# Kernel tuning notes

Hardware: AMD Instinct MI355X
Metric: run time of the kernel (lower is better)

Reference implementation:

```python
import jax, jax.numpy as jnp
import numpy as np

HID = 2048   # hidden_size
NH = 32      # num_heads (== num_kv_heads)
HD = 64      # head_dim
TH, TW = 8, 16     # tile sizes (tile numel 128, flex-attention block)
WH, WW = 16, 32    # window sizes in tokens
SCALE = 1.0 / np.sqrt(HD)


def _kv_tile_index(h_dim, w_dim):
    # Static tile-level sliding window (mirrors sliding_window_tile_2d mask_mod).
    Ht, Wt = h_dim // TH, w_dim // TW          # tile grid
    wh, ww = WH // TH, WW // TW                # window in tile units
    lr, rr = wh // 2, wh // 2 + (wh % 2 - 1)
    lc, rc = ww // 2, ww // 2 + (ww % 2 - 1)
    cr = np.clip(np.arange(Ht), lr, Ht - 1 - rr)   # clamped window center rows
    cc = np.clip(np.arange(Wt), lc, Wt - 1 - rc)
    rows = cr[:, None] + np.arange(-lr, rr + 1)[None, :]   # [Ht, wh]
    cols = cc[:, None] + np.arange(-lc, rc + 1)[None, :]   # [Wt, ww]
    idx = rows[:, None, :, None] * Wt + cols[None, :, None, :]  # [Ht,Wt,wh,ww]
    return idx.reshape(Ht * Wt, wh * ww)


def _tile_order(x, h_dim, w_dim):
    # seq layout (nth th ntw tw) -> [B, NH, n_tiles, TH*TW, HD]  (the einops rearrange)
    B, S, _ = x.shape
    nth, ntw = h_dim // TH, w_dim // TW
    x = x.reshape(B, nth, TH, ntw, TW, NH, HD)
    x = x.transpose(0, 5, 1, 3, 2, 4, 6)  # b h nth ntw th tw d
    return x.reshape(B, NH, nth * ntw, TH * TW, HD)


def setup_inputs() -> dict:
    key = jax.random.key(0)
    ks = jax.random.split(key, 5)
    B, hd, wd = 2, 64, 64
    S = hd * wd
    sc = 1.0 / np.sqrt(HID)
    return {
        "hidden_states": jax.random.normal(ks[0], (B, S, HID), jnp.float32),
        "Wq": jax.random.normal(ks[1], (HID, NH * HD), jnp.float32) * sc,
        "Wk": jax.random.normal(ks[2], (HID, NH * HD), jnp.float32) * sc,
        "Wv": jax.random.normal(ks[3], (HID, NH * HD), jnp.float32) * sc,
        "Wo": jax.random.normal(ks[4], (NH * HD, HID), jnp.float32) * sc,
        "h_dim": hd,
        "w_dim": wd,
    }


def reference(hidden_states, Wq, Wk, Wv, Wo, h_dim, w_dim):
    B, S, _ = hidden_states.shape
    q = _tile_order(hidden_states @ Wq, h_dim, w_dim)
    k = _tile_order(hidden_states @ Wk, h_dim, w_dim)
    v = _tile_order(hidden_states @ Wv, h_dim, w_dim)
    kv_tiles = jnp.asarray(_kv_tile_index(h_dim, w_dim))  # [T, nw] static
    T, nw = kv_tiles.shape
    tn = TH * TW
    # gather the allowed kv tiles per query tile (block-sparse structure)
    kg = k[:, :, kv_tiles].reshape(B, NH, T, nw * tn, HD)
    vg = v[:, :, kv_tiles].reshape(B, NH, T, nw * tn, HD)
    s = jnp.einsum('bhtqd,bhtkd->bhtqk', q, kg) * SCALE  # [B,H,T,128,nw*128]
    p = jax.nn.softmax(s, axis=-1)
    o = jnp.einsum('bhtqk,bhtkd->bhtqd', p, vg)
    # back to (nth th ntw tw) token order, then output projection
    nth, ntw = h_dim // TH, w_dim // TW
    o = o.reshape(B, NH, nth, ntw, TH, TW, HD)
    o = o.transpose(0, 2, 4, 3, 5, 1, 6).reshape(B, S, NH * HD)
    return o @ Wo
```

## Files before the change

kernel.cpp:

```cpp
#include <hip/hip_runtime.h>
#include <math.h>

typedef _Float16 f16;
typedef _Float16 f16x8 __attribute__((ext_vector_type(8)));
typedef float f32x4 __attribute__((ext_vector_type(4)));

#define K_HID 2048
#define N_SEQ 4096
#define N_BATCH 2
#define M_ROWS 8192

__device__ __forceinline__ void gl2lds16(const f16* g, f16* l) {
  auto gp = (const __attribute__((address_space(1))) unsigned*)(unsigned long long)(uintptr_t)g;
  auto lp = (__attribute__((address_space(3))) unsigned*)(unsigned)(uintptr_t)l;
  __builtin_amdgcn_global_load_lds(gp, lp, 16, 0, 0);
}

__global__ __launch_bounds__(256) void cvt_f32_to_f16(const float* __restrict__ x,
                                                      f16* __restrict__ y, int n) {
  int i = (blockIdx.x * 256 + threadIdx.x) * 8;
  if (i >= n) return;
  float4 a = *(const float4*)(x + i);
  float4 b = *(const float4*)(x + i + 4);
  f16x8 o;
  o[0] = (f16)a.x; o[1] = (f16)a.y; o[2] = (f16)a.z; o[3] = (f16)a.w;
  o[4] = (f16)b.x; o[5] = (f16)b.y; o[6] = (f16)b.z; o[7] = (f16)b.w;
  *(f16x8*)(y + i) = o;
}

__global__ __launch_bounds__(256) void transpose_cvt(const float* __restrict__ W0,
                                                     const float* __restrict__ W1,
                                                     const float* __restrict__ W2,
                                                     const float* __restrict__ W3,
                                                     f16* __restrict__ WT) {
  const float* W = (blockIdx.z == 0) ? W0 : (blockIdx.z == 1) ? W1
                 : (blockIdx.z == 2) ? W2 : W3;
  f16* Wt = WT + (size_t)blockIdx.z * K_HID * K_HID;
  __shared__ float tile[32][33];
  int bx = blockIdx.x * 32;
  int by = blockIdx.y * 32;
  int x = threadIdx.x & 31;
  int y = threadIdx.x >> 5;
  for (int i = 0; i < 32; i += 8)
    tile[y + i][x] = W[(size_t)(by + y + i) * K_HID + bx + x];
  __syncthreads();
  for (int i = 0; i < 32; i += 8)
    Wt[(size_t)(bx + y + i) * K_HID + by + x] = (f16)tile[x][y + i];
}

template <typename OutT>
__global__ __launch_bounds__(512, 2) void gemm_bt(const f16* __restrict__ A,
                                                  const f16* __restrict__ BtBase,
                                                  OutT* __restrict__ CBase,
                                                  int M, int N, int Kd,
                                                  size_t bzStride, size_t czStride) {
  const f16* Bt = BtBase + bzStride * blockIdx.z;
  OutT* C = CBase + czStride * blockIdx.z;
  __shared__ f16 sA[2][256 * 64];
  __shared__ f16 sB[2][256 * 64];
  int tid = threadIdx.x;
  int lane = tid & 63, wave = tid >> 6;
  int quad = lane >> 4, l16 = lane & 15;
  int mBase = blockIdx.y * 256, nBase = blockIdx.x * 256;
  int wm = (wave >> 2) * 128, wn = (wave & 3) * 64;

  f32x4 acc[8][4];
#pragma unroll
  for (int mf = 0; mf < 8; mf++)
#pragma unroll
    for (int nf = 0; nf < 4; nf++) acc[mf][nf] = (f32x4){0.f, 0.f, 0.f, 0.f};

  int r8 = lane >> 3;
  int csw = ((lane & 7) ^ r8) * 8;
  const f16* Ag = A + (size_t)(mBase + wave * 32 + r8) * Kd + csw;
  const f16* Bg = Bt + (size_t)(nBase + wave * 32 + r8) * Kd + csw;

  f16* lA0 = &sA[0][wave * 2048];
  f16* lA1 = &sA[1][wave * 2048];
  f16* lB0 = &sB[0][wave * 2048];
  f16* lB1 = &sB[1][wave * 2048];

#define STAGE_A(dst, t)                                                  \
  { _Pragma("unroll") for (int q = 0; q < 4; ++q)                        \
      gl2lds16(Ag + (size_t)(q * 8) * Kd + (size_t)(t) * 64, (dst) + q * 512); }
#define STAGE_B(dst, t)                                                  \
  { _Pragma("unroll") for (int q = 0; q < 4; ++q)                        \
      gl2lds16(Bg + (size_t)(q * 8) * Kd + (size_t)(t) * 64, (dst) + q * 512); }

  int aRow = (wm + l16) * 64;
  int bRow = (wn + l16) * 64;
  int c0 = (quad ^ (l16 & 7)) * 8;
  int c1 = c0 ^ 32;

  const int NT = Kd >> 6;
  STAGE_A(lA0, 0);
  STAGE_B(lB0, 0);

  const f16* sAc = &sA[0][0]; const f16* sAo = &sA[1][0];
  const f16* sBc = &sB[0][0]; const f16* sBo = &sB[1][0];
  f16* lAn = lA1; f16* lAo = lA0;
  f16* lBn = lB1; f16* lBo = lB0;

  for (int t = 0; t < NT; ++t) {
    if (t + 1 < NT) {
      STAGE_A(lAn, t + 1);
      asm volatile("s_waitcnt vmcnt(4)" ::: "memory");
    } else {
      asm volatile("s_waitcnt vmcnt(0)" ::: "memory");
    }
    __builtin_amdgcn_s_barrier();
    __builtin_amdgcn_sched_barrier(0);

    f16x8 bf[4][2], af[4][2];
#pragma unroll
    for (int nf = 0; nf < 4; nf++) {
      bf[nf][0] = *(const f16x8*)&sBc[bRow + nf * 1024 + c0];
      bf[nf][1] = *(const f16x8*)&sBc[bRow + nf * 1024 + c1];
    }
#pragma unroll
    for (int mf = 0; mf < 4; mf++) {
      af[mf][0] = *(const f16x8*)&sAc[aRow + mf * 1024 + c0];
      af[mf][1] = *(const f16x8*)&sAc[aRow + mf * 1024 + c1];
    }
    __builtin_amdgcn_s_setprio(1);
#pragma unroll
    for (int mf = 0; mf < 4; mf++)
#pragma unroll
      for (int nf = 0; nf < 4; nf++) {
        acc[mf][nf] = __builtin_amdgcn_mfma_f32_16x16x32_f16(af[mf][0], bf[nf][0], acc[mf][nf], 0, 0, 0);
        acc[mf][nf] = __builtin_amdgcn_mfma_f32_16x16x32_f16(af[mf][1], bf[nf][1], acc[mf][nf], 0, 0, 0);
      }
    __builtin_amdgcn_s_setprio(0);

    if (t + 1 < NT) STAGE_B(lBn, t + 1);

#pragma unroll
    for (int mf = 0; mf < 4; mf++) {
      af[mf][0] = *(const f16x8*)&sAc[aRow + 4096 + mf * 1024 + c0];
      af[mf][1] = *(const f16x8*)&sAc[aRow + 4096 + mf * 1024 + c1];
    }
    __builtin_amdgcn_s_setprio(1);
#pragma unroll
    for (int mf = 0; mf < 4; mf++)
#pragma unroll
      for (int nf = 0; nf < 4; nf++) {
        acc[mf + 4][nf] = __builtin_amdgcn_mfma_f32_16x16x32_f16(af[mf][0], bf[nf][0], acc[mf + 4][nf], 0, 0, 0);
        acc[mf + 4][nf] = __builtin_amdgcn_mfma_f32_16x16x32_f16(af[mf][1], bf[nf][1], acc[mf + 4][nf], 0, 0, 0);
      }
    __builtin_amdgcn_s_setprio(0);
    __builtin_amdgcn_sched_barrier(0);
    __builtin_amdgcn_s_barrier();

    { const f16* tt;
      tt = sAc; sAc = sAo; sAo = tt;
      tt = sBc; sBc = sBo; sBo = tt; }
    { f16* tt;
      tt = lAn; lAn = lAo; lAo = tt;
      tt = lBn; lBn = lBo; lBo = tt; }
  }
#undef STAGE_A
#undef STAGE_B

#pragma unroll
  for (int mf = 0; mf < 8; mf++) {
    int row = mBase + wm + mf * 16 + quad * 4;
#pragma unroll
    for (int nf = 0; nf < 4; nf++) {
      int col = nBase + wn + nf * 16 + l16;
      OutT* Cp = C + (size_t)row * N + col;
#pragma unroll
      for (int r = 0; r < 4; r++) Cp[(size_t)r * N] = (OutT)acc[mf][nf][r];
    }
  }
}

__global__ __launch_bounds__(256) void attn_kernel(const f16* __restrict__ Q,
                                                   const f16* __restrict__ Kg,
                                                   const f16* __restrict__ V,
                                                   f16* __restrict__ O) {
  __shared__ f16 sQ[128 * 72];
  __shared__ f16 sK[64 * 72];
  __shared__ f16 sVt[64 * 72];
  __shared__ f16 sP[128 * 72];

  int t = blockIdx.x, h = blockIdx.y, b = blockIdx.z;
  int nth_i = t >> 2, ntw_i = t & 3;
  int tid = threadIdx.x;
  int lane = tid & 63, wave = tid >> 6;
  int quad = lane >> 4, l16 = lane & 15;
  const size_t bstride = (size_t)N_SEQ * K_HID;
  const f16* Qb = Q + (size_t)b * bstride + h * 64;
  const f16* Kb = Kg + (size_t)b * bstride + h * 64;
  const f16* Vb = V + (size_t)b * bstride + h * 64;

  const float SC2 = 0.18033688f;

  for (int i = tid; i < 1024; i += 256) {
    int qr = i >> 3, dc = (i & 7) * 8;
    int s = (nth_i * 8 + (qr >> 4)) * 64 + ntw_i * 16 + (qr & 15);
    *(float4*)&sQ[qr * 72 + dc] = *(const float4*)&Qb[(size_t)s * K_HID + dc];
  }
  __syncthreads();

  f16x8 qf[2][2];
#pragma unroll
  for (int qs = 0; qs < 2; qs++)
#pragma unroll
    for (int kk = 0; kk < 2; kk++)
      qf[qs][kk] = *(const f16x8*)&sQ[(wave * 32 + qs * 16 + l16) * 72 + kk * 32 + quad * 8];

  f32x4 oacc[2][4];
#pragma unroll
  for (int qs = 0; qs < 2; qs++)
#pragma unroll
    for (int dt = 0; dt < 4; dt++) oacc[qs][dt] = (f32x4){0.f, 0.f, 0.f, 0.f};
  float mrow[2][4], lrow[2][4];
#pragma unroll
  for (int qs = 0; qs < 2; qs++)
#pragma unroll
    for (int r = 0; r < 4; r++) { mrow[qs][r] = -1e30f; lrow[qs][r] = 0.f; }

  int cr = min(max(nth_i, 1), 7);
  int cc = min(max(ntw_i, 1), 3);

  for (int c = 0; c < 8; c++) {
    int kt = c >> 1, half = c & 1;
    int ti = cr - 1 + (kt >> 1), tj = cc - 1 + (kt & 1);
    for (int i = tid; i < 512; i += 256) {
      int kl = i >> 3, dc = (i & 7) * 8;
      int kr = half * 64 + kl;
      int s = (ti * 8 + (kr >> 4)) * 64 + tj * 16 + (kr & 15);
      *(float4*)&sK[kl * 72 + dc] = *(const float4*)&Kb[(size_t)s * K_HID + dc];
      f16x8 vv = *(const f16x8*)&Vb[(size_t)s * K_HID + dc];
      int sw = kl ^ dc;
#pragma unroll
      for (int j = 0; j < 8; j++) sVt[(dc + j) * 72 + sw] = vv[j];
    }
    __syncthreads();

    f32x4 sacc[2][4];
#pragma unroll
    for (int qs = 0; qs < 2; qs++)
#pragma unroll
      for (int ks = 0; ks < 4; ks++) sacc[qs][ks] = (f32x4){0.f, 0.f, 0.f, 0.f};
#pragma unroll
    for (int ks = 0; ks < 4; ks++) {
      f16x8 kf0 = *(const f16x8*)&sK[(ks * 16 + l16) * 72 + quad * 8];
      f16x8 kf1 = *(const f16x8*)&sK[(ks * 16 + l16) * 72 + 32 + quad * 8];
#pragma unroll
      for (int qs = 0; qs < 2; qs++) {
        sacc[qs][ks] = __builtin_amdgcn_mfma_f32_16x16x32_f16(qf[qs][0], kf0, sacc[qs][ks], 0, 0, 0);
        sacc[qs][ks] = __builtin_amdgcn_mfma_f32_16x16x32_f16(qf[qs][1], kf1, sacc[qs][ks], 0, 0, 0);
      }
    }

#pragma unroll
    for (int qs = 0; qs < 2; qs++) {
#pragma unroll
      for (int r = 0; r < 4; r++) {
        float mx = fmaxf(fmaxf(sacc[qs][0][r], sacc[qs][1][r]),
                         fmaxf(sacc[qs][2][r], sacc[qs][3][r]));
        for (int d = 1; d < 16; d <<= 1) mx = fmaxf(mx, __shfl_xor(mx, d, 64));
        mx *= SC2;
        float mold = mrow[qs][r];
        float mnew = fmaxf(mold, mx);
        mrow[qs][r] = mnew;
        float alpha = exp2f(mold - mnew);
        lrow[qs][r] *= alpha;
#pragma unroll
        for (int dt = 0; dt < 4; dt++) oacc[qs][dt][r] *= alpha;
      }
#pragma unroll
      for (int ks = 0; ks < 4; ks++) {
#pragma unroll
        for (int r = 0; r < 4; r++) {
          float p = exp2f(sacc[qs][ks][r] * SC2 - mrow[qs][r]);
          lrow[qs][r] += p;
          sP[(wave * 32 + qs * 16 + quad * 4 + r) * 72 + ks * 16 + l16] = (f16)p;
        }
      }
    }
    __syncthreads();

#pragma unroll
    for (int kk = 0; kk < 2; kk++) {
      f16x8 pf[2];
#pragma unroll
      for (int qs = 0; qs < 2; qs++)
        pf[qs] = *(const f16x8*)&sP[(wave * 32 + qs * 16 + l16) * 72 + kk * 32 + quad * 8];
#pragma unroll
      for (int dt = 0; dt < 4; dt++) {
        int d = dt * 16 + l16;
        f16x8 vf = *(const f16x8*)&sVt[d * 72 + ((kk * 32 + quad * 8) ^ (d & 56))];
#pragma unroll
        for (int qs = 0; qs < 2; qs++)
          oacc[qs][dt] = __builtin_amdgcn_mfma_f32_16x16x32_f16(pf[qs], vf, oacc[qs][dt], 0, 0, 0);
      }
    }
    __syncthreads();
  }

  f16* Ob = O + (size_t)b * bstride + h * 64;
#pragma unroll
  for (int qs = 0; qs < 2; qs++) {
#pragma unroll
    for (int r = 0; r < 4; r++) {
      float l = lrow[qs][r];
      for (int d = 1; d < 16; d <<= 1) l += __shfl_xor(l, d, 64);
      float inv = 1.0f / l;
      int qr = wave * 32 + qs * 16 + quad * 4 + r;
      int s = (nth_i * 8 + (qr >> 4)) * 64 + ntw_i * 16 + (qr & 15);
#pragma unroll
      for (int dt = 0; dt < 4; dt++)
        Ob[(size_t)s * K_HID + dt * 16 + l16] = (f16)(oacc[qs][dt][r] * inv);
    }
  }
}

extern "C" void kernel_launch(void* const* d_in, const int* in_sizes, int n_in,
                              void* d_out, int out_size, void* d_ws, size_t ws_size,
                              hipStream_t stream) {
  const float* hs = (const float*)d_in[0];
  const float* Wq = (const float*)d_in[1];
  const float* Wk = (const float*)d_in[2];
  const float* Wv = (const float*)d_in[3];
  const float* Wo = (const float*)d_in[4];
  float* out = (float*)d_out;

  char* ws = (char*)d_ws;
  const size_t WELEM = (size_t)K_HID * K_HID;
  const size_t XELEM = (size_t)M_ROWS * K_HID;
  f16* WT = (f16*)ws;  ws += 4 * WELEM * sizeof(f16);
  f16* Xh = (f16*)ws;  ws += XELEM * sizeof(f16);
  f16* Qb = (f16*)ws;  ws += XELEM * sizeof(f16);
  f16* Kb = (f16*)ws;  ws += XELEM * sizeof(f16);
  f16* Vb = (f16*)ws;  ws += XELEM * sizeof(f16);
  f16* Ob = (f16*)ws;  ws += XELEM * sizeof(f16);

  cvt_f32_to_f16<<<(int)(XELEM / (256 * 8)), 256, 0, stream>>>(hs, Xh, (int)XELEM);
  transpose_cvt<<<dim3(64, 64, 4), 256, 0, stream>>>(Wq, Wk, Wv, Wo, WT);
  gemm_bt<f16><<<dim3(8, 32, 3), 512, 0, stream>>>(Xh, WT, Qb, M_ROWS, K_HID, K_HID,
                                                   WELEM, XELEM);
  attn_kernel<<<dim3(32, 32, 2), 256, 0, stream>>>(Qb, Kb, Vb, Ob);
  gemm_bt<float><<<dim3(8, 32, 1), 512, 0, stream>>>(Ob, WT + 3 * WELEM, out,
                                                     M_ROWS, K_HID, K_HID, 0, 0);
}
```

Baseline: 560.1 us.

## Restructure GEMM main loop into four-phase K-split pipeline with interleaved staging

Changes the GEMM's LDS layout from 64-wide swizzled rows to two 32-wide K halves. The main loop now runs four MFMA phases per K tile, each separated by barriers, with the next tile's A and B halves issued between phases so loads overlap compute more finely. The A fragments for all 8 m-fragments are held in registers, and B is reloaded in halves. The unswizzled 32-wide rows may cause LDS bank conflicts, and the extra barriers add synchronisation cost.

```diff
diff --git a/kernel.cpp b/kernel.cpp
--- a/kernel.cpp
+++ b/kernel.cpp
@@ -56,8 +56,8 @@
                                                   size_t bzStride, size_t czStride) {
   const f16* Bt = BtBase + bzStride * blockIdx.z;
   OutT* C = CBase + czStride * blockIdx.z;
-  __shared__ f16 sA[2][256 * 64];
-  __shared__ f16 sB[2][256 * 64];
+  __shared__ f16 sA[2 * 2 * 256 * 32];
+  __shared__ f16 sB[2 * 2 * 256 * 32];
   int tid = threadIdx.x;
   int lane = tid & 63, wave = tid >> 6;
   int quad = lane >> 4, l16 = lane & 15;
@@ -70,96 +70,101 @@
 #pragma unroll
     for (int nf = 0; nf < 4; nf++) acc[mf][nf] = (f32x4){0.f, 0.f, 0.f, 0.f};
 
-  int r8 = lane >> 3;
-  int csw = ((lane & 7) ^ r8) * 8;
-  const f16* Ag = A + (size_t)(mBase + wave * 32 + r8) * Kd + csw;
-  const f16* Bg = Bt + (size_t)(nBase + wave * 32 + r8) * Kd + csw;
-
-  f16* lA0 = &sA[0][wave * 2048];
-  f16* lA1 = &sA[1][wave * 2048];
-  f16* lB0 = &sB[0][wave * 2048];
-  f16* lB1 = &sB[1][wave * 2048];
-
-#define STAGE_A(dst, t)                                                  \
-  { _Pragma("unroll") for (int q = 0; q < 4; ++q)                        \
-      gl2lds16(Ag + (size_t)(q * 8) * Kd + (size_t)(t) * 64, (dst) + q * 512); }
-#define STAGE_B(dst, t)                                                  \
-  { _Pragma("unroll") for (int q = 0; q < 4; ++q)                        \
-      gl2lds16(Bg + (size_t)(q * 8) * Kd + (size_t)(t) * 64, (dst) + q * 512); }
-
-  int aRow = (wm + l16) * 64;
-  int bRow = (wn + l16) * 64;
-  int c0 = (quad ^ (l16 & 7)) * 8;
-  int c1 = c0 ^ 32;
+  int r4 = lane >> 2;
+  int kc = (lane & 3) * 8;
+  const f16* Ag = A + (size_t)(mBase + wave * 16 + r4) * Kd + kc;
+  const f16* Bg = Bt + (size_t)(nBase + wave * 16 + r4) * Kd + kc;
+
+#define STG(g, dstBase, kh, j, tt)                                           \
+  gl2lds16((g) + (size_t)((j) * 128) * Kd + (size_t)((tt) * 64 + (kh) * 32), \
+           (dstBase) + (kh) * 8192 + ((j) * 128 + wave * 16) * 32)
+
+  f16* cA = sA;          f16* nA = sA + 16384;
+  f16* cB = sB;          f16* nB = sB + 16384;
 
   const int NT = Kd >> 6;
-  STAGE_A(lA0, 0);
-  STAGE_B(lB0, 0);
-
-  const f16* sAc = &sA[0][0]; const f16* sAo = &sA[1][0];
-  const f16* sBc = &sB[0][0]; const f16* sBo = &sB[1][0];
-  f16* lAn = lA1; f16* lAo = lA0;
-  f16* lBn = lB1; f16* lBo = lB0;
+
+  STG(Ag, cA, 0, 0, 0); STG(Ag, cA, 0, 1, 0);
+  STG(Bg, cB, 0, 0, 0); STG(Bg, cB, 0, 1, 0);
+  STG(Ag, cA, 1, 0, 0); STG(Ag, cA, 1, 1, 0);
+  STG(Bg, cB, 1, 0, 0); STG(Bg, cB, 1, 1, 0);
+  asm volatile("s_waitcnt vmcnt(4)" ::: "memory");
+  __builtin_amdgcn_s_barrier();
+
+  int aOff = (wm + l16) * 32 + quad * 8;
+  int bOff = (wn + l16) * 32 + quad * 8;
 
   for (int t = 0; t < NT; ++t) {
-    if (t + 1 < NT) {
-      STAGE_A(lAn, t + 1);
-      asm volatile("s_waitcnt vmcnt(4)" ::: "memory");
-    } else {
-      asm volatile("s_waitcnt vmcnt(0)" ::: "memory");
-    }
-    __builtin_amdgcn_s_barrier();
+    const bool pre = (t + 1 < NT);
+    f16x8 af[8], bq[2];
+#pragma unroll
+    for (int mf = 0; mf < 8; mf++) af[mf] = *(const f16x8*)&cA[aOff + mf * 512];
+#pragma unroll
+    for (int nf = 0; nf < 2; nf++) bq[nf] = *(const f16x8*)&cB[bOff + nf * 512];
+    if (pre) { STG(Ag, nA, 0, 0, t + 1); STG(Ag, nA, 0, 1, t + 1); }
+    __builtin_amdgcn_s_barrier();
+    asm volatile("s_waitcnt lgkmcnt(0)" ::: "memory");
     __builtin_amdgcn_sched_barrier(0);
-
-    f16x8 bf[4][2], af[4][2];
-#pragma unroll
-    for (int nf = 0; nf < 4; nf++) {
-      bf[nf][0] = *(const f16x8*)&sBc[bRow + nf * 1024 + c0];
-      bf[nf][1] = *(const f16x8*)&sBc[bRow + nf * 1024 + c1];
-    }
-#pragma unroll
-    for (int mf = 0; mf < 4; mf++) {
-      af[mf][0] = *(const f16x8*)&sAc[aRow + mf * 1024 + c0];
-      af[mf][1] = *(const f16x8*)&sAc[aRow + mf * 1024 + c1];
-    }
     __builtin_amdgcn_s_setprio(1);
 #pragma unroll
-    for (int mf = 0; mf < 4; mf++)
-#pragma unroll
-      for (int nf = 0; nf < 4; nf++) {
-        acc[mf][nf] = __builtin_amdgcn_mfma_f32_16x16x32_f16(af[mf][0], bf[nf][0], acc[mf][nf], 0, 0, 0);
-        acc[mf][nf] = __builtin_amdgcn_mfma_f32_16x16x32_f16(af[mf][1], bf[nf][1], acc[mf][nf], 0, 0, 0);
-      }
+    for (int mf = 0; mf < 8; mf++)
+#pragma unroll
+      for (int nf = 0; nf < 2; nf++)
+        acc[mf][nf] = __builtin_amdgcn_mfma_f32_16x16x32_f16(af[mf], bq[nf], acc[mf][nf], 0, 0, 0);
     __builtin_amdgcn_s_setprio(0);
-
-    if (t + 1 < NT) STAGE_B(lBn, t + 1);
-
-#pragma unroll
-    for (int mf = 0; mf < 4; mf++) {
-      af[mf][0] = *(const f16x8*)&sAc[aRow + 4096 + mf * 1024 + c0];
-      af[mf][1] = *(const f16x8*)&sAc[aRow + 4096 + mf * 1024 + c1];
-    }
+    __builtin_amdgcn_s_barrier();
+#pragma unroll
+    for (int nf = 0; nf < 2; nf++) bq[nf] = *(const f16x8*)&cB[bOff + (nf + 2) * 512];
+    if (pre) { STG(Bg, nB, 0, 0, t + 1); STG(Bg, nB, 0, 1, t + 1); }
+    __builtin_amdgcn_s_barrier();
+    asm volatile("s_waitcnt lgkmcnt(0)" ::: "memory");
+    __builtin_amdgcn_sched_barrier(0);
     __builtin_amdgcn_s_setprio(1);
 #pragma unroll
-    for (int mf = 0; mf < 4; mf++)
-#pragma unroll
-      for (int nf = 0; nf < 4; nf++) {
-        acc[mf + 4][nf] = __builtin_amdgcn_mfma_f32_16x16x32_f16(af[mf][0], bf[nf][0], acc[mf + 4][nf], 0, 0, 0);
-        acc[mf + 4][nf] = __builtin_amdgcn_mfma_f32_16x16x32_f16(af[mf][1], bf[nf][1], acc[mf + 4][nf], 0, 0, 0);
-      }
+    for (int mf = 0; mf < 8; mf++)
+#pragma unroll
+      for (int nf = 0; nf < 2; nf++)
+        acc[mf][nf + 2] = __builtin_amdgcn_mfma_f32_16x16x32_f16(af[mf], bq[nf], acc[mf][nf + 2], 0, 0, 0);
     __builtin_amdgcn_s_setprio(0);
+    __builtin_amdgcn_s_barrier();
+    if (pre) asm volatile("s_waitcnt vmcnt(4)" ::: "memory");
+    else     asm volatile("s_waitcnt vmcnt(0)" ::: "memory");
+#pragma unroll
+    for (int mf = 0; mf < 8; mf++) af[mf] = *(const f16x8*)&cA[8192 + aOff + mf * 512];
+#pragma unroll
+    for (int nf = 0; nf < 2; nf++) bq[nf] = *(const f16x8*)&cB[8192 + bOff + (nf + 2) * 512];
+    if (pre) { STG(Ag, nA, 1, 0, t + 1); STG(Ag, nA, 1, 1, t + 1); }
+    __builtin_amdgcn_s_barrier();
+    asm volatile("s_waitcnt lgkmcnt(0)" ::: "memory");
     __builtin_amdgcn_sched_barrier(0);
-    __builtin_amdgcn_s_barrier();
-
-    { const f16* tt;
-      tt = sAc; sAc = sAo; sAo = tt;
-      tt = sBc; sBc = sBo; sBo = tt; }
-    { f16* tt;
-      tt = lAn; lAn = lAo; lAo = tt;
-      tt = lBn; lBn = lBo; lBo = tt; }
-  }
-#undef STAGE_A
-#undef STAGE_B
+    __builtin_amdgcn_s_setprio(1);
+#pragma unroll
+    for (int mf = 0; mf < 8; mf++)
+#pragma unroll
+      for (int nf = 0; nf < 2; nf++)
+        acc[mf][nf + 2] = __builtin_amdgcn_mfma_f32_16x16x32_f16(af[mf], bq[nf], acc[mf][nf + 2], 0, 0, 0);
+    __builtin_amdgcn_s_setprio(0);
+    __builtin_amdgcn_s_barrier();
+#pragma unroll
+    for (int nf = 0; nf < 2; nf++) bq[nf] = *(const f16x8*)&cB[8192 + bOff + nf * 512];
+    if (pre) { STG(Bg, nB, 1, 0, t + 1); STG(Bg, nB, 1, 1, t + 1); }
+    if (pre) asm volatile("s_waitcnt vmcnt(4)" ::: "memory");
+    else     asm volatile("s_waitcnt vmcnt(0)" ::: "memory");
+    __builtin_amdgcn_s_barrier();
+    asm volatile("s_waitcnt lgkmcnt(0)" ::: "memory");
+    __builtin_amdgcn_sched_barrier(0);
+    __builtin_amdgcn_s_setprio(1);
+#pragma unroll
+    for (int mf = 0; mf < 8; mf++)
+#pragma unroll
+      for (int nf = 0; nf < 2; nf++)
+        acc[mf][nf] = __builtin_amdgcn_mfma_f32_16x16x32_f16(af[mf], bq[nf], acc[mf][nf], 0, 0, 0);
+    __builtin_amdgcn_s_setprio(0);
+    __builtin_amdgcn_s_barrier();
+    f16* tA = cA; cA = nA; nA = tA;
+    f16* tB = cB; cB = nB; nB = tB;
+  }
+#undef STG
 
 #pragma unroll
   for (int mf = 0; mf < 8; mf++) {
```

Result: slower. 594.4 us (+6.1%).

## Transpose attention MFMA operands so softmax rows live per lane

Applied to the files above, without the earlier changes.

Swaps the A/B operands of the QK^T and PV MFMAs so each lane holds a query column rather than a row slice. Row max and sum then need only two cross-quad shuffles instead of four-step reductions per register, and P and O can be written as packed f16x4 vectors. The Q staging buffer is merged into the P buffer to save LDS, and the V transpose now writes packed f16x2 pairs. The change targets the attention kernel only; the GEMMs dominate total time, so the overall effect may be small.

```diff
diff --git a/kernel.cpp b/kernel.cpp
--- a/kernel.cpp
+++ b/kernel.cpp
@@ -2,6 +2,8 @@
 #include <math.h>
 
 typedef _Float16 f16;
+typedef _Float16 f16x2 __attribute__((ext_vector_type(2)));
+typedef _Float16 f16x4 __attribute__((ext_vector_type(4)));
 typedef _Float16 f16x8 __attribute__((ext_vector_type(8)));
 typedef float f32x4 __attribute__((ext_vector_type(4)));
 
@@ -178,10 +180,9 @@
                                                    const f16* __restrict__ Kg,
                                                    const f16* __restrict__ V,
                                                    f16* __restrict__ O) {
-  __shared__ f16 sQ[128 * 72];
   __shared__ f16 sK[64 * 72];
   __shared__ f16 sVt[64 * 72];
-  __shared__ f16 sP[128 * 72];
+  __shared__ f16 sPt[128 * 72];
 
   int t = blockIdx.x, h = blockIdx.y, b = blockIdx.z;
   int nth_i = t >> 2, ntw_i = t & 3;
@@ -198,7 +199,7 @@
   for (int i = tid; i < 1024; i += 256) {
     int qr = i >> 3, dc = (i & 7) * 8;
     int s = (nth_i * 8 + (qr >> 4)) * 64 + ntw_i * 16 + (qr & 15);
-    *(float4*)&sQ[qr * 72 + dc] = *(const float4*)&Qb[(size_t)s * K_HID + dc];
+    *(float4*)&sPt[qr * 72 + dc] = *(const float4*)&Qb[(size_t)s * K_HID + dc];
   }
   __syncthreads();
 
@@ -207,18 +208,15 @@
   for (int qs = 0; qs < 2; qs++)
 #pragma unroll
     for (int kk = 0; kk < 2; kk++)
-      qf[qs][kk] = *(const f16x8*)&sQ[(wave * 32 + qs * 16 + l16) * 72 + kk * 32 + quad * 8];
+      qf[qs][kk] = *(const f16x8*)&sPt[(wave * 32 + qs * 16 + l16) * 72 + kk * 32 + quad * 8];
 
   f32x4 oacc[2][4];
 #pragma unroll
   for (int qs = 0; qs < 2; qs++)
 #pragma unroll
     for (int dt = 0; dt < 4; dt++) oacc[qs][dt] = (f32x4){0.f, 0.f, 0.f, 0.f};
-  float mrow[2][4], lrow[2][4];
-#pragma unroll
-  for (int qs = 0; qs < 2; qs++)
-#pragma unroll
-    for (int r = 0; r < 4; r++) { mrow[qs][r] = -1e30f; lrow[qs][r] = 0.f; }
+  float mrow[2] = {-1e30f, -1e30f};
+  float lrow[2] = {0.f, 0.f};
 
   int cr = min(max(nth_i, 1), 7);
   int cc = min(max(ntw_i, 1), 3);
@@ -231,10 +229,21 @@
       int kr = half * 64 + kl;
       int s = (ti * 8 + (kr >> 4)) * 64 + tj * 16 + (kr & 15);
       *(float4*)&sK[kl * 72 + dc] = *(const float4*)&Kb[(size_t)s * K_HID + dc];
-      f16x8 vv = *(const f16x8*)&Vb[(size_t)s * K_HID + dc];
-      int sw = kl ^ dc;
-#pragma unroll
-      for (int j = 0; j < 8; j++) sVt[(dc + j) * 72 + sw] = vv[j];
+    }
+    {
+      int pr = tid >> 3, dc = (tid & 7) * 8;
+      int k0 = pr * 2;
+      int kr0 = half * 64 + k0, kr1 = kr0 + 1;
+      int s0 = (ti * 8 + (kr0 >> 4)) * 64 + tj * 16 + (kr0 & 15);
+      int s1 = (ti * 8 + (kr1 >> 4)) * 64 + tj * 16 + (kr1 & 15);
+      f16x8 v0 = *(const f16x8*)&Vb[(size_t)s0 * K_HID + dc];
+      f16x8 v1 = *(const f16x8*)&Vb[(size_t)s1 * K_HID + dc];
+      int swc = k0 ^ dc;
+#pragma unroll
+      for (int j = 0; j < 8; j++) {
+        f16x2 pv; pv[0] = v0[j]; pv[1] = v1[j];
+        *(f16x2*)&sVt[(dc + j) * 72 + swc] = pv;
+      }
     }
     __syncthreads();
 
@@ -249,36 +258,44 @@
       f16x8 kf1 = *(const f16x8*)&sK[(ks * 16 + l16) * 72 + 32 + quad * 8];
 #pragma unroll
       for (int qs = 0; qs < 2; qs++) {
-        sacc[qs][ks] = __builtin_amdgcn_mfma_f32_16x16x32_f16(qf[qs][0], kf0, sacc[qs][ks], 0, 0, 0);
-        sacc[qs][ks] = __builtin_amdgcn_mfma_f32_16x16x32_f16(qf[qs][1], kf1, sacc[qs][ks], 0, 0, 0);
+        sacc[qs][ks] = __builtin_amdgcn_mfma_f32_16x16x32_f16(kf0, qf[qs][0], sacc[qs][ks], 0, 0, 0);
+        sacc[qs][ks] = __builtin_amdgcn_mfma_f32_16x16x32_f16(kf1, qf[qs][1], sacc[qs][ks], 0, 0, 0);
       }
     }
 
 #pragma unroll
     for (int qs = 0; qs < 2; qs++) {
-#pragma unroll
-      for (int r = 0; r < 4; r++) {
-        float mx = fmaxf(fmaxf(sacc[qs][0][r], sacc[qs][1][r]),
-                         fmaxf(sacc[qs][2][r], sacc[qs][3][r]));
-        for (int d = 1; d < 16; d <<= 1) mx = fmaxf(mx, __shfl_xor(mx, d, 64));
-        mx *= SC2;
-        float mold = mrow[qs][r];
-        float mnew = fmaxf(mold, mx);
-        mrow[qs][r] = mnew;
-        float alpha = exp2f(mold - mnew);
-        lrow[qs][r] *= alpha;
-#pragma unroll
-        for (int dt = 0; dt < 4; dt++) oacc[qs][dt][r] *= alpha;
-      }
+      float mx = sacc[qs][0][0];
+#pragma unroll
+      for (int ks = 0; ks < 4; ks++)
+#pragma unroll
+        for (int r = 0; r < 4; r++) mx = fmaxf(mx, sacc[qs][ks][r]);
+      mx = fmaxf(mx, __shfl_xor(mx, 16, 64));
+      mx = fmaxf(mx, __shfl_xor(mx, 32, 64));
+      mx *= SC2;
+      float mold = mrow[qs];
+      float mnew = fmaxf(mold, mx);
+      mrow[qs] = mnew;
+      float alpha = exp2f(mold - mnew);
+      lrow[qs] *= alpha;
+#pragma unroll
+      for (int dt = 0; dt < 4; dt++)
+#pragma unroll
+        for (int r = 0; r < 4; r++) oacc[qs][dt][r] *= alpha;
+      float ls = 0.f;
+      int qrow = (wave * 32 + qs * 16 + l16) * 72;
 #pragma unroll
       for (int ks = 0; ks < 4; ks++) {
+        f16x4 pk;
 #pragma unroll
         for (int r = 0; r < 4; r++) {
-          float p = exp2f(sacc[qs][ks][r] * SC2 - mrow[qs][r]);
-          lrow[qs][r] += p;
-          sP[(wave * 32 + qs * 16 + quad * 4 + r) * 72 + ks * 16 + l16] = (f16)p;
+          float p = exp2f(sacc[qs][ks][r] * SC2 - mnew);
+          ls += p;
+          pk[r] = (f16)p;
         }
-      }
+        *(f16x4*)&sPt[qrow + ks * 16 + quad * 4] = pk;
+      }
+      lrow[qs] += ls;
     }
     __syncthreads();
 
@@ -287,14 +304,14 @@
       f16x8 pf[2];
 #pragma unroll
       for (int qs = 0; qs < 2; qs++)
-        pf[qs] = *(const f16x8*)&sP[(wave * 32 + qs * 16 + l16) * 72 + kk * 32 + quad * 8];
+        pf[qs] = *(const f16x8*)&sPt[(wave * 32 + qs * 16 + l16) * 72 + kk * 32 + quad * 8];
 #pragma unroll
       for (int dt = 0; dt < 4; dt++) {
         int d = dt * 16 + l16;
         f16x8 vf = *(const f16x8*)&sVt[d * 72 + ((kk * 32 + quad * 8) ^ (d & 56))];
 #pragma unroll
         for (int qs = 0; qs < 2; qs++)
-          oacc[qs][dt] = __builtin_amdgcn_mfma_f32_16x16x32_f16(pf[qs], vf, oacc[qs][dt], 0, 0, 0);
+          oacc[qs][dt] = __builtin_amdgcn_mfma_f32_16x16x32_f16(vf, pf[qs], oacc[qs][dt], 0, 0, 0);
       }
     }
     __syncthreads();
@@ -303,16 +320,18 @@
   f16* Ob = O + (size_t)b * bstride + h * 64;
 #pragma unroll
   for (int qs = 0; qs < 2; qs++) {
-#pragma unroll
-    for (int r = 0; r < 4; r++) {
-      float l = lrow[qs][r];
-      for (int d = 1; d < 16; d <<= 1) l += __shfl_xor(l, d, 64);
-      float inv = 1.0f / l;
-      int qr = wave * 32 + qs * 16 + quad * 4 + r;
-      int s = (nth_i * 8 + (qr >> 4)) * 64 + ntw_i * 16 + (qr & 15);
-#pragma unroll
-      for (int dt = 0; dt < 4; dt++)
-        Ob[(size_t)s * K_HID + dt * 16 + l16] = (f16)(oacc[qs][dt][r] * inv);
+    float l = lrow[qs];
+    l += __shfl_xor(l, 16, 64);
+    l += __shfl_xor(l, 32, 64);
+    float inv = 1.0f / l;
+    int q = wave * 32 + qs * 16 + l16;
+    int s = (nth_i * 8 + (q >> 4)) * 64 + ntw_i * 16 + (q & 15);
+#pragma unroll
+    for (int dt = 0; dt < 4; dt++) {
+      f16x4 ok;
+#pragma unroll
+      for (int r = 0; r < 4; r++) ok[r] = (f16)(oacc[qs][dt][r] * inv);
+      *(f16x4*)&Ob[(size_t)s * K_HID + dt * 16 + quad * 4] = ok;
     }
   }
 }
```

Result: faster. 524.8 us (-6.3%).
